# Optimization experiments

Hardware: AMD Instinct MI355X
Metric: run time of the kernel (lower is better)

The kernel has to match this reference:

```python
import jax, jax.numpy as jnp
import numpy as np

B, S, D = 2, 1024, 4096
N_HEADS, KV_HEADS, HEAD_DIM = 32, 8, 128
EPS = 1e-6
ROPE_THETA = 1e6


def setup_inputs() -> dict:
    key = jax.random.key(0)
    ks = jax.random.split(key, 7)
    scale = 0.02
    x = jax.random.normal(ks[0], (B, S, D), dtype=jnp.float32)
    positions = jnp.broadcast_to(jnp.arange(S, dtype=jnp.int32)[None, :], (B, S))
    wq = jax.random.normal(ks[1], (D, N_HEADS, HEAD_DIM), dtype=jnp.float32) * scale
    wk = jax.random.normal(ks[2], (D, KV_HEADS, HEAD_DIM), dtype=jnp.float32) * scale
    wv = jax.random.normal(ks[3], (D, KV_HEADS, HEAD_DIM), dtype=jnp.float32) * scale
    wo = jax.random.normal(ks[4], (N_HEADS, HEAD_DIM, D), dtype=jnp.float32) * scale
    q_norm_w = 1.0 + jax.random.normal(ks[5], (HEAD_DIM,), dtype=jnp.float32) * 0.01
    k_norm_w = 1.0 + jax.random.normal(ks[6], (HEAD_DIM,), dtype=jnp.float32) * 0.01
    return {"x": x, "positions": positions, "wq": wq, "wk": wk, "wv": wv,
            "wo": wo, "q_norm_w": q_norm_w, "k_norm_w": k_norm_w}


def _rms_norm(t, w):
    # per-head RMSNorm over last (head_dim) axis
    var = jnp.mean(jnp.square(t), axis=-1, keepdims=True)
    return (t * jax.lax.rsqrt(var + EPS)) * w


def _rope(t, positions):
    # neox-style rotary embedding; t: [B, S, n, H], positions: [B, S]
    half = t.shape[-1] // 2
    inv_freq = 1.0 / (ROPE_THETA ** (jnp.arange(0, half, dtype=jnp.float32) / half))
    ang = positions.astype(jnp.float32)[..., None] * inv_freq  # [B, S, half]
    cos = jnp.cos(ang)[:, :, None, :]  # [B, S, 1, half]
    sin = jnp.sin(ang)[:, :, None, :]
    t1, t2 = t[..., :half], t[..., half:]
    return jnp.concatenate([t1 * cos - t2 * sin, t2 * cos + t1 * sin], axis=-1)


def reference(x, positions, wq, wk, wv, wo, q_norm_w, k_norm_w):
    # QKV projections (einsum layers: 'bsd,dnh->bsnh')
    q = jnp.einsum('bsd,dnh->bsnh', x, wq)  # [B, S, N, H]
    k = jnp.einsum('bsd,dkh->bskh', x, wk)  # [B, S, K, H]
    v = jnp.einsum('bsd,dkh->bskh', x, wv)
    # per-head QK RMSNorm, then RoPE
    q = _rope(_rms_norm(q, q_norm_w), positions)
    k = _rope(_rms_norm(k, k_norm_w), positions)
    # GQA: expand KV heads to query heads
    groups = N_HEADS // KV_HEADS
    k = jnp.repeat(k, groups, axis=2)  # [B, S, N, H]
    v = jnp.repeat(v, groups, axis=2)
    sm_scale = HEAD_DIM ** -0.5
    scores = jnp.einsum('bqnh,btnh->bnqt', q, k) * sm_scale  # [B, N, S, S]
    causal = jnp.tril(jnp.ones((S, S), dtype=bool))
    scores = jnp.where(causal[None, None], scores, jnp.finfo(scores.dtype).min)
    probs = jax.nn.softmax(scores, axis=-1)
    attn = jnp.einsum('bnqt,btnh->bqnh', probs, v)  # [B, S, N, H]
    out = jnp.einsum('bqnh,nhd->bqd', attn, wo)  # output projection
    return out
```

## Files before the change

kernel.cpp:

```cpp
#include <hip/hip_runtime.h>
#include <stdint.h>

#define S_LEN   1024
#define D_MODEL 4096
#define NHQ     32
#define NKV     8
#define HD      128
#define NTOK    2048
#define NQKV    6144
#define SM_SCALE 0.08838834764831843f
#define LOG2E    1.4426950408889634f

typedef __attribute__((ext_vector_type(8))) __bf16 bf16x8;
typedef __attribute__((ext_vector_type(4))) float f32x4;

__device__ __forceinline__ unsigned short f2bf(float f) {
  union { float f; unsigned u; } x; x.f = f;
  unsigned r = x.u + 0x7fffu + ((x.u >> 16) & 1u);
  return (unsigned short)(r >> 16);
}
__device__ __forceinline__ float bf2f(unsigned short u) {
  union { unsigned u; float f; } x; x.u = (unsigned)u << 16; return x.f;
}

__device__ __forceinline__ void gload_lds16(const void* g, void* l) {
  __builtin_amdgcn_global_load_lds((__attribute__((address_space(1))) void*)g,
                                   (__attribute__((address_space(3))) void*)l,
                                   16, 0, 0);
}

__global__ void k_f32_to_bf16(const float* __restrict__ in,
                              unsigned short* __restrict__ out, int n8) {
  int i = blockIdx.x * blockDim.x + threadIdx.x;
  if (i >= n8) return;
  const float4* p = (const float4*)(in + (size_t)i * 8);
  float4 v0 = p[0], v1 = p[1];
  uint4 o;
  o.x = f2bf(v0.x) | ((unsigned)f2bf(v0.y) << 16);
  o.y = f2bf(v0.z) | ((unsigned)f2bf(v0.w) << 16);
  o.z = f2bf(v1.x) | ((unsigned)f2bf(v1.y) << 16);
  o.w = f2bf(v1.z) | ((unsigned)f2bf(v1.w) << 16);
  *(uint4*)(out + (size_t)i * 8) = o;
}

__global__ void k_transpose(const float* __restrict__ in,
                            unsigned short* __restrict__ out, int R, int C) {
  __shared__ float t[32][33];
  int c = threadIdx.x & 31, r0 = threadIdx.x >> 5;
  int cb = blockIdx.x * 32, rb = blockIdx.y * 32;
#pragma unroll
  for (int i = 0; i < 4; ++i) {
    int r = r0 + i * 8;
    t[r][c] = in[(size_t)(rb + r) * C + cb + c];
  }
  __syncthreads();
#pragma unroll
  for (int i = 0; i < 4; ++i) {
    int r = r0 + i * 8;
    out[(size_t)(cb + r) * R + rb + c] = f2bf(t[c][r]);
  }
}


#define LGKM0 { asm volatile("s_waitcnt lgkmcnt(0)" ::: "memory"); \
                __builtin_amdgcn_sched_barrier(0); }
#define SCHED __builtin_amdgcn_sched_barrier(0);
#define BAR   __builtin_amdgcn_s_barrier();
#define GATE  { if constexpr (NF == 4)                                          \
                  asm volatile("s_waitcnt vmcnt(4)" ::: "memory");              \
                else                                                            \
                  asm volatile("s_waitcnt vmcnt(3)" ::: "memory"); }

#define STGA(h, bufb, kOff)                                                     \
  _Pragma("unroll")                                                             \
  for (int i_ = 0; i_ < 2; ++i_)                                                \
    gload_lds16(gA[i_] + (kOff) + (h) * 64,                                     \
                smem + (bufb) + (h) * 16384 + dA[i_]);

#define STGB(h, bufb, kOff)                                                     \
  _Pragma("unroll")                                                             \
  for (int i_ = 0; i_ < NF / 2; ++i_)                                           \
    gload_lds16(gB[i_] + (kOff) + (h) * 64,                                     \
                smem + (bufb) + 32768 + (h) * (NF * 4096) + dB[i_]);

#define RD_A(dst, mh, kh, bufb)                                                 \
  _Pragma("unroll")                                                             \
  for (int mf = 0; mf < 4; ++mf) {                                              \
    int row = wr * 128 + (mh) * 64 + mf * 16 + lr;                              \
    dst[mf] = *(const bf16x8*)(smem + (bufb) + (kh) * 16384 + row * 64          \
                               + ((lg * 16) ^ (((row >> 1) & 3) << 4)));        \
  }

#define RD_B(dst, kh, bufb)                                                     \
  _Pragma("unroll")                                                             \
  for (int nf = 0; nf < NF; ++nf) {                                             \
    int row = wc * (NF * 16) + nf * 16 + lr;                                    \
    dst[nf] = *(const bf16x8*)(smem + (bufb) + 32768 + (kh) * (NF * 4096)       \
                               + row * 64 + ((lg * 16) ^ (((row >> 1) & 3) << 4))); \
  }

#define MFMA16(mh, AF, BF)                                                      \
  __builtin_amdgcn_s_setprio(1);                                                \
  _Pragma("unroll")                                                             \
  for (int mf = 0; mf < 4; ++mf)                                                \
    _Pragma("unroll")                                                           \
    for (int nf = 0; nf < NF; ++nf)                                             \
      acc[(mh) * 4 + mf][nf] = __builtin_amdgcn_mfma_f32_16x16x32_bf16(         \
          AF[mf], BF[nf], acc[(mh) * 4 + mf][nf], 0, 0, 0);                     \
  __builtin_amdgcn_s_setprio(0);

template <int NF, typename OutT>
__global__ __launch_bounds__(512, 1) void k_gemm256(
    const unsigned short* __restrict__ Aptr,
    const unsigned short* __restrict__ Bptr,
    OutT* __restrict__ C,
    int Kstride, int ldc, int NT, int SGN, int nxn) {
  extern __shared__ __align__(16) char smem[];
  constexpr int BUFST = 32768 + NF * 8192;
  int tid = threadIdx.x;
  int l = tid & 63;
  int w = tid >> 6;
  int lr = l & 15, lg = l >> 4;
  int wr = w >> 2, wc = w & 3;
  int per_xcd = gridDim.x >> 3;
  int x8 = blockIdx.x & 7, i = blockIdx.x >> 3;
  int SGM = per_xcd / SGN;
  int xr = x8 / nxn, xc = x8 - xr * nxn;
  int iy = i / SGN;
  int by = xr * SGM + iy, bx = xc * SGN + (i - iy * SGN);
  int bm = by * 256, bn = bx * (NF * 64);

  const char* gA[2]; int dA[2];
#pragma unroll
  for (int i_ = 0; i_ < 2; ++i_) {
    int lin = i_ * 512 + tid;
    int r_ = lin >> 2, slot = lin & 3, sw = slot ^ ((r_ >> 1) & 3);
    gA[i_] = (const char*)(Aptr + (size_t)(bm + r_) * Kstride) + sw * 16;
    dA[i_] = lin * 16;
  }
  const char* gB[NF / 2]; int dB[NF / 2];
#pragma unroll
  for (int i_ = 0; i_ < NF / 2; ++i_) {
    int lin = i_ * 512 + tid;
    int r_ = lin >> 2, slot = lin & 3, sw = slot ^ ((r_ >> 1) & 3);
    gB[i_] = (const char*)(Bptr + (size_t)(bn + r_) * Kstride) + sw * 16;
    dB[i_] = lin * 16;
  }

  f32x4 acc[8][NF] = {};
  bf16x8 afA[4], afB[4], bfA[NF], bfB[NF];

  STGA(0, 0, 0) STGB(0, 0, 0)
  STGA(1, 0, 0) STGB(1, 0, 0)
  GATE
  BAR
  RD_A(afA, 0, 0, 0) RD_B(bfA, 0, 0)

  for (int kt = 0; kt < NT; ++kt) {
    int curb = (kt & 1) * BUFST;
    int nxtb = BUFST - curb;
    int kOff = (kt + 1) * 128;
    STGA(0, nxtb, kOff)
    BAR LGKM0
    RD_A(afB, 1, 0, curb) SCHED
    MFMA16(0, afA, bfA)
    BAR
    STGB(0, nxtb, kOff)
    GATE BAR LGKM0
    RD_A(afA, 0, 1, curb) RD_B(bfB, 1, curb) SCHED
    MFMA16(1, afB, bfA)
    BAR
    STGA(1, nxtb, kOff)
    BAR LGKM0
    RD_A(afB, 1, 1, curb) SCHED
    MFMA16(0, afA, bfB)
    BAR
    STGB(1, nxtb, kOff)
    GATE BAR LGKM0
    RD_A(afA, 0, 0, nxtb) RD_B(bfA, 0, nxtb) SCHED
    MFMA16(1, afB, bfB)
    BAR
  }

#pragma unroll
  for (int mh = 0; mh < 2; ++mh)
#pragma unroll
    for (int mf = 0; mf < 4; ++mf)
#pragma unroll
      for (int nf = 0; nf < NF; ++nf)
#pragma unroll
        for (int j = 0; j < 4; ++j) {
          size_t idx = (size_t)(bm + wr * 128 + mh * 64 + mf * 16 + lg * 4 + j) * ldc +
                       bn + wc * (NF * 16) + nf * 16 + lr;
          float v = acc[mh * 4 + mf][nf][j];
          if constexpr (sizeof(OutT) == 2) C[idx] = f2bf(v);
          else C[idx] = v;
        }
}

__global__ void k_norm_rope(const unsigned short* __restrict__ qkv,
                            const float* __restrict__ w,
                            const int* __restrict__ positions,
                            unsigned short* __restrict__ out, int nheads, int colbase,
                            float oscale) {
  int wid = blockIdx.x * 4 + (threadIdx.x >> 6);
  int lane = threadIdx.x & 63;
  int token = wid / nheads, head = wid - token * nheads;
  const unsigned short* src = qkv + (size_t)token * NQKV + colbase + head * HD;
  float e0 = bf2f(src[lane]), e1 = bf2f(src[lane + 64]);
  float ss = e0 * e0 + e1 * e1;
#pragma unroll
  for (int m = 1; m < 64; m <<= 1) ss += __shfl_xor(ss, m, 64);
  float rs = rsqrtf(ss * (1.0f / 128.0f) + 1e-6f);
  float n0 = e0 * rs * w[lane], n1 = e1 * rs * w[lane + 64];
  int pos = positions[token];
  float invf = exp2f((float)lane * (-19.931568569324174f / 64.0f));
  float ang = (float)pos * invf;
  float sv, cv;
  sincosf(ang, &sv, &cv);
  float o0 = (n0 * cv - n1 * sv) * oscale;
  float o1 = (n1 * cv + n0 * sv) * oscale;
  int b = token >> 10, s = token & 1023;
  size_t ob = ((size_t)(b * nheads + head) * S_LEN + s) * HD;
  out[ob + lane] = f2bf(o0);
  out[ob + 64 + lane] = f2bf(o1);
}

__global__ void k_v_transpose(const unsigned short* __restrict__ qkv,
                              unsigned short* __restrict__ vt) {
  __shared__ unsigned short t[32][33];
  int slice = blockIdx.z;
  int b = slice >> 3, kh = slice & 7;
  const unsigned short* in = qkv + (size_t)(b * S_LEN) * NQKV + 5120 + kh * HD;
  unsigned short* out = vt + (size_t)slice * HD * S_LEN;
  int c = threadIdx.x & 31, r0 = threadIdx.x >> 5;
  int s0 = blockIdx.y * 32, d0 = blockIdx.x * 32;
#pragma unroll
  for (int i = 0; i < 4; ++i) {
    int r = r0 + i * 8;
    t[r][c] = in[(size_t)(s0 + r) * NQKV + d0 + c];
  }
  __syncthreads();
#pragma unroll
  for (int i = 0; i < 4; ++i) {
    int r = r0 + i * 8;
    out[(size_t)(d0 + r) * S_LEN + s0 + c] = t[c][r];
  }
}

__global__ __launch_bounds__(512) void k_attn(const unsigned short* __restrict__ qh,
                                              const unsigned short* __restrict__ kbuf,
                                              const unsigned short* __restrict__ vtbuf,
                                              unsigned short* __restrict__ attn_out) {
  __shared__ __align__(16) unsigned short k_lds[64 * 128];
  __shared__ __align__(16) unsigned short v_lds[128 * 64];
  __shared__ __align__(16) unsigned short p_lds[8][16 * 64];
  int b = blockIdx.z, h = blockIdx.y, bx = blockIdx.x;
  int khd = h >> 2;
  int tid = threadIdx.x, w = tid >> 6, l = tid & 63;
  int lr = l & 15, lg = l >> 4;
  const unsigned short* K = kbuf + (size_t)(b * NKV + khd) * S_LEN * HD;
  const unsigned short* VT = vtbuf + (size_t)(b * NKV + khd) * HD * S_LEN;
  char* klp = (char*)k_lds;
  char* vlp = (char*)v_lds;
  char* plp = (char*)p_lds[w];
  int swz = (lr & 7) << 4;

  for (int strip = 0; strip < 2; ++strip) {
    int qs = strip ? (7 - bx) : bx;
    int q0 = qs * 128;
    int rbase = q0 + w * 16;
    const unsigned short* Q = qh + ((size_t)(b * NHQ + h) * S_LEN + rbase) * HD;
    bf16x8 qf[4];
#pragma unroll
    for (int kk = 0; kk < 4; ++kk)
      qf[kk] = *(const bf16x8*)&Q[(size_t)lr * HD + kk * 32 + lg * 8];

    f32x4 o[8] = {};
    float m_[4], l_[4];
#pragma unroll
    for (int j = 0; j < 4; ++j) { m_[j] = -1e30f; l_[j] = 0.0f; }

    int nt = 2 * qs + 2;
    for (int t = 0; t < nt; ++t) {
      int t0 = t * 64;
      __syncthreads();
#pragma unroll
      for (int it = 0; it < 2; ++it) {
        int db = (tid + it * 512) * 16;
        int kr = db >> 8, kc = db & 255;
        gload_lds16(K + (size_t)(t0 + kr) * HD + ((kc ^ ((kr & 7) << 4)) >> 1), klp + db);
        int vr = db >> 7, vc = db & 127;
        gload_lds16(VT + (size_t)vr * S_LEN + t0 + ((vc ^ ((vr & 7) << 4)) >> 1), vlp + db);
      }
      __syncthreads();

      f32x4 sc[4];
      __builtin_amdgcn_s_setprio(1);
#pragma unroll
      for (int ct = 0; ct < 4; ++ct) {
        f32x4 s = {};
        int row = ct * 16 + lr;
#pragma unroll
        for (int kk = 0; kk < 4; ++kk) {
          bf16x8 kf = *(const bf16x8*)(klp + row * 256 + ((kk * 64 + lg * 16) ^ swz));
          s = __builtin_amdgcn_mfma_f32_16x16x32_bf16(qf[kk], kf, s, 0, 0, 0);
        }
        sc[ct] = s;
      }
      __builtin_amdgcn_s_setprio(0);

      bool fullw = (t0 + 63 <= rbase);
      float alpha[4];
#pragma unroll
      for (int j = 0; j < 4; ++j) {
        if (!fullw) {
          int rg = rbase + lg * 4 + j;
#pragma unroll
          for (int ct = 0; ct < 4; ++ct)
            sc[ct][j] = (t0 + ct * 16 + lr <= rg) ? sc[ct][j] : -1e30f;
        }
        float mx = fmaxf(fmaxf(sc[0][j], sc[1][j]), fmaxf(sc[2][j], sc[3][j]));
#pragma unroll
        for (int msk = 1; msk < 16; msk <<= 1) mx = fmaxf(mx, __shfl_xor(mx, msk, 64));
        float mn = fmaxf(m_[j], mx);
        alpha[j] = exp2f(m_[j] - mn);
        int q = lg * 4 + j;
        int psw = (q & 7) << 4;
        float ps = 0.0f;
#pragma unroll
        for (int ct = 0; ct < 4; ++ct) {
          float p = exp2f(sc[ct][j] - mn);
          ps += p;
          *(unsigned short*)(plp + q * 128 + (((ct * 16 + lr) * 2) ^ psw)) = f2bf(p);
        }
#pragma unroll
        for (int msk = 1; msk < 16; msk <<= 1) ps += __shfl_xor(ps, msk, 64);
        l_[j] = l_[j] * alpha[j] + ps;
        m_[j] = mn;
      }
#pragma unroll
      for (int dc = 0; dc < 8; ++dc) {
        o[dc][0] *= alpha[0]; o[dc][1] *= alpha[1];
        o[dc][2] *= alpha[2]; o[dc][3] *= alpha[3];
      }
      asm volatile("s_waitcnt lgkmcnt(0)" ::: "memory");
      __builtin_amdgcn_s_setprio(1);
#pragma unroll
      for (int kt = 0; kt < 2; ++kt) {
        bf16x8 pa = *(const bf16x8*)(plp + lr * 128 + ((kt * 64 + lg * 16) ^ swz));
#pragma unroll
        for (int dc = 0; dc < 8; ++dc) {
          int vrow = dc * 16 + lr;
          bf16x8 vf = *(const bf16x8*)(vlp + vrow * 128 + ((kt * 64 + lg * 16) ^ swz));
          o[dc] = __builtin_amdgcn_mfma_f32_16x16x32_bf16(pa, vf, o[dc], 0, 0, 0);
        }
      }
      __builtin_amdgcn_s_setprio(0);
    }

#pragma unroll
    for (int j = 0; j < 4; ++j) {
      int rg = rbase + lg * 4 + j;
      size_t row = (size_t)(b * S_LEN + rg) * D_MODEL + h * HD;
      float inv = 1.0f / l_[j];
#pragma unroll
      for (int dc = 0; dc < 8; ++dc)
        attn_out[row + dc * 16 + lr] = f2bf(o[dc][j] * inv);
    }
  }
}

extern "C" void kernel_launch(void* const* d_in, const int* in_sizes, int n_in,
                              void* d_out, int out_size, void* d_ws, size_t ws_size,
                              hipStream_t stream) {
  const float* x        = (const float*)d_in[0];
  const int* positions  = (const int*)d_in[1];
  const float* wq       = (const float*)d_in[2];
  const float* wk       = (const float*)d_in[3];
  const float* wv       = (const float*)d_in[4];
  const float* wo       = (const float*)d_in[5];
  const float* qnw      = (const float*)d_in[6];
  const float* knw      = (const float*)d_in[7];
  float* out            = (float*)d_out;

  char* ws = (char*)d_ws;
  unsigned short* xb   = (unsigned short*)(ws);
  unsigned short* wB   = (unsigned short*)(ws + 16777216);
  unsigned short* woT  = (unsigned short*)(ws + 67108864);
  unsigned short* qkvb = (unsigned short*)(ws + 100663296);
  unsigned short* qh   = wB;
  unsigned short* khb  = (unsigned short*)(ws + 33554432);
  unsigned short* vtb  = (unsigned short*)(ws + 37748736);
  unsigned short* attn = xb;

  dim3 tb(256);
  k_f32_to_bf16<<<4096, tb, 0, stream>>>(x, xb, 1048576);
  k_transpose<<<dim3(128, 128), tb, 0, stream>>>(wq, wB, 4096, 4096);
  k_transpose<<<dim3(32, 128), tb, 0, stream>>>(wk, wB + (size_t)4096 * 4096, 4096, 1024);
  k_transpose<<<dim3(32, 128), tb, 0, stream>>>(wv, wB + (size_t)5120 * 4096, 4096, 1024);
  k_transpose<<<dim3(128, 128), tb, 0, stream>>>(wo, woT, 4096, 4096);

  k_gemm256<4, unsigned short><<<dim3(192), dim3(512), 131072, stream>>>(
      xb, wB, qkvb, 4096, 6144, 64, 6, 4);

  k_norm_rope<<<16384, tb, 0, stream>>>(qkvb, qnw, positions, qh, 32, 0, SM_SCALE * LOG2E);
  k_norm_rope<<<4096, tb, 0, stream>>>(qkvb, knw, positions, khb, 8, 4096, 1.0f);
  k_v_transpose<<<dim3(4, 32, 16), tb, 0, stream>>>(qkvb, vtb);

  k_attn<<<dim3(4, 32, 2), dim3(512), 0, stream>>>(qh, khb, vtb, attn);

  k_gemm256<2, float><<<dim3(256), dim3(512), 98304, stream>>>(
      attn, woT, out, 4096, 4096, 64, 8, 4);
}
```

Baseline: 331.8 us.

## Fuse prep and norm kernels, split-K the output projection with NF=4 tiles

Merges the x conversion and the four weight transposes into a single launch, and merges the Q/K norm-rope kernels with the V transpose into another. The output projection switches to 256x256 tiles split across two K halves, with the second half written to an fp32 partial buffer and summed by a new reduce kernel. The aim is fewer kernel launches and a better tile shape for the final GEMM, at the cost of extra partial-buffer traffic and an added reduction pass. The K-loop prefetch offset is also clamped so the last iteration does not read past its K range.

```diff
diff --git a/kernel.cpp b/kernel.cpp
--- a/kernel.cpp
+++ b/kernel.cpp
@@ -29,25 +29,33 @@
                                    16, 0, 0);
 }
 
-__global__ void k_f32_to_bf16(const float* __restrict__ in,
-                              unsigned short* __restrict__ out, int n8) {
-  int i = blockIdx.x * blockDim.x + threadIdx.x;
-  if (i >= n8) return;
-  const float4* p = (const float4*)(in + (size_t)i * 8);
-  float4 v0 = p[0], v1 = p[1];
-  uint4 o;
-  o.x = f2bf(v0.x) | ((unsigned)f2bf(v0.y) << 16);
-  o.y = f2bf(v0.z) | ((unsigned)f2bf(v0.w) << 16);
-  o.z = f2bf(v1.x) | ((unsigned)f2bf(v1.y) << 16);
-  o.w = f2bf(v1.z) | ((unsigned)f2bf(v1.w) << 16);
-  *(uint4*)(out + (size_t)i * 8) = o;
-}
-
-__global__ void k_transpose(const float* __restrict__ in,
-                            unsigned short* __restrict__ out, int R, int C) {
+__global__ void k_prep(const float* __restrict__ x,
+                       const float* __restrict__ wq, const float* __restrict__ wk,
+                       const float* __restrict__ wv, const float* __restrict__ wo,
+                       unsigned short* __restrict__ xb,
+                       unsigned short* __restrict__ wB,
+                       unsigned short* __restrict__ woT) {
   __shared__ float t[32][33];
-  int c = threadIdx.x & 31, r0 = threadIdx.x >> 5;
-  int cb = blockIdx.x * 32, rb = blockIdx.y * 32;
+  int bx = blockIdx.x, by = blockIdx.y, tid = threadIdx.x;
+  if (bx >= 320) {
+    int i = ((bx - 320) * 128 + by) * 256 + tid;
+    const float4* p = (const float4*)(x + (size_t)i * 8);
+    float4 v0 = p[0], v1 = p[1];
+    uint4 o;
+    o.x = f2bf(v0.x) | ((unsigned)f2bf(v0.y) << 16);
+    o.y = f2bf(v0.z) | ((unsigned)f2bf(v0.w) << 16);
+    o.z = f2bf(v1.x) | ((unsigned)f2bf(v1.y) << 16);
+    o.w = f2bf(v1.z) | ((unsigned)f2bf(v1.w) << 16);
+    *(uint4*)(xb + (size_t)i * 8) = o;
+    return;
+  }
+  const float* in; unsigned short* out; int C, tbx;
+  if (bx < 128)      { in = wq; out = wB;                          C = 4096; tbx = bx; }
+  else if (bx < 160) { in = wk; out = wB + (size_t)4096 * 4096;    C = 1024; tbx = bx - 128; }
+  else if (bx < 192) { in = wv; out = wB + (size_t)5120 * 4096;    C = 1024; tbx = bx - 160; }
+  else               { in = wo; out = woT;                         C = 4096; tbx = bx - 192; }
+  int c = tid & 31, r0 = tid >> 5;
+  int cb = tbx * 32, rb = by * 32;
 #pragma unroll
   for (int i = 0; i < 4; ++i) {
     int r = r0 + i * 8;
@@ -57,7 +65,7 @@
 #pragma unroll
   for (int i = 0; i < 4; ++i) {
     int r = r0 + i * 8;
-    out[(size_t)(cb + r) * R + rb + c] = f2bf(t[c][r]);
+    out[(size_t)(cb + r) * 4096 + rb + c] = f2bf(t[c][r]);
   }
 }
 
@@ -113,8 +121,8 @@
 __global__ __launch_bounds__(512, 1) void k_gemm256(
     const unsigned short* __restrict__ Aptr,
     const unsigned short* __restrict__ Bptr,
-    OutT* __restrict__ C,
-    int Kstride, int ldc, int NT, int SGN, int nxn) {
+    OutT* __restrict__ C, float* __restrict__ Cpart,
+    int Kstride, int ldc, int NT, int SGN, int nxn, int nps) {
   extern __shared__ __align__(16) char smem[];
   constexpr int BUFST = 32768 + NF * 8192;
   int tid = threadIdx.x;
@@ -122,20 +130,23 @@
   int w = tid >> 6;
   int lr = l & 15, lg = l >> 4;
   int wr = w >> 2, wc = w & 3;
-  int per_xcd = gridDim.x >> 3;
-  int x8 = blockIdx.x & 7, i = blockIdx.x >> 3;
+  int ks = (blockIdx.x >= nps) ? 1 : 0;
+  int bid = blockIdx.x - ks * nps;
+  int per_xcd = nps >> 3;
+  int x8 = bid & 7, i = bid >> 3;
   int SGM = per_xcd / SGN;
   int xr = x8 / nxn, xc = x8 - xr * nxn;
   int iy = i / SGN;
   int by = xr * SGM + iy, bx = xc * SGN + (i - iy * SGN);
   int bm = by * 256, bn = bx * (NF * 64);
+  int k0e = ks * NT * 64;
 
   const char* gA[2]; int dA[2];
 #pragma unroll
   for (int i_ = 0; i_ < 2; ++i_) {
     int lin = i_ * 512 + tid;
     int r_ = lin >> 2, slot = lin & 3, sw = slot ^ ((r_ >> 1) & 3);
-    gA[i_] = (const char*)(Aptr + (size_t)(bm + r_) * Kstride) + sw * 16;
+    gA[i_] = (const char*)(Aptr + (size_t)(bm + r_) * Kstride + k0e) + sw * 16;
     dA[i_] = lin * 16;
   }
   const char* gB[NF / 2]; int dB[NF / 2];
@@ -143,7 +154,7 @@
   for (int i_ = 0; i_ < NF / 2; ++i_) {
     int lin = i_ * 512 + tid;
     int r_ = lin >> 2, slot = lin & 3, sw = slot ^ ((r_ >> 1) & 3);
-    gB[i_] = (const char*)(Bptr + (size_t)(bn + r_) * Kstride) + sw * 16;
+    gB[i_] = (const char*)(Bptr + (size_t)(bn + r_) * Kstride + k0e) + sw * 16;
     dB[i_] = lin * 16;
   }
 
@@ -159,7 +170,8 @@
   for (int kt = 0; kt < NT; ++kt) {
     int curb = (kt & 1) * BUFST;
     int nxtb = BUFST - curb;
-    int kOff = (kt + 1) * 128;
+    int kcl = (kt + 1 < NT) ? kt + 1 : NT - 1;
+    int kOff = kcl * 128;
     STGA(0, nxtb, kOff)
     BAR LGKM0
     RD_A(afB, 1, 0, curb) SCHED
@@ -193,58 +205,82 @@
           size_t idx = (size_t)(bm + wr * 128 + mh * 64 + mf * 16 + lg * 4 + j) * ldc +
                        bn + wc * (NF * 16) + nf * 16 + lr;
           float v = acc[mh * 4 + mf][nf][j];
-          if constexpr (sizeof(OutT) == 2) C[idx] = f2bf(v);
+          if (ks) Cpart[idx] = v;
+          else if constexpr (sizeof(OutT) == 2) C[idx] = f2bf(v);
           else C[idx] = v;
         }
 }
 
-__global__ void k_norm_rope(const unsigned short* __restrict__ qkv,
-                            const float* __restrict__ w,
-                            const int* __restrict__ positions,
-                            unsigned short* __restrict__ out, int nheads, int colbase,
-                            float oscale) {
-  int wid = blockIdx.x * 4 + (threadIdx.x >> 6);
-  int lane = threadIdx.x & 63;
-  int token = wid / nheads, head = wid - token * nheads;
-  const unsigned short* src = qkv + (size_t)token * NQKV + colbase + head * HD;
-  float e0 = bf2f(src[lane]), e1 = bf2f(src[lane + 64]);
-  float ss = e0 * e0 + e1 * e1;
-#pragma unroll
-  for (int m = 1; m < 64; m <<= 1) ss += __shfl_xor(ss, m, 64);
-  float rs = rsqrtf(ss * (1.0f / 128.0f) + 1e-6f);
-  float n0 = e0 * rs * w[lane], n1 = e1 * rs * w[lane + 64];
-  int pos = positions[token];
-  float invf = exp2f((float)lane * (-19.931568569324174f / 64.0f));
-  float ang = (float)pos * invf;
-  float sv, cv;
-  sincosf(ang, &sv, &cv);
-  float o0 = (n0 * cv - n1 * sv) * oscale;
-  float o1 = (n1 * cv + n0 * sv) * oscale;
-  int b = token >> 10, s = token & 1023;
-  size_t ob = ((size_t)(b * nheads + head) * S_LEN + s) * HD;
-  out[ob + lane] = f2bf(o0);
-  out[ob + 64 + lane] = f2bf(o1);
-}
-
-__global__ void k_v_transpose(const unsigned short* __restrict__ qkv,
-                              unsigned short* __restrict__ vt) {
-  __shared__ unsigned short t[32][33];
-  int slice = blockIdx.z;
+__global__ void k_reduce_add(float* __restrict__ out, const float* __restrict__ p,
+                             int n4) {
+  int i = blockIdx.x * blockDim.x + threadIdx.x;
+  int stride = gridDim.x * blockDim.x;
+  for (; i < n4; i += stride) {
+    float4 a = ((const float4*)out)[i];
+    float4 b = ((const float4*)p)[i];
+    a.x += b.x; a.y += b.y; a.z += b.z; a.w += b.w;
+    ((float4*)out)[i] = a;
+  }
+}
+
+__global__ void k_norm_vt(const unsigned short* __restrict__ qkv,
+                          const float* __restrict__ qw,
+                          const float* __restrict__ kw,
+                          const int* __restrict__ positions,
+                          unsigned short* __restrict__ qh,
+                          unsigned short* __restrict__ khb,
+                          unsigned short* __restrict__ vt,
+                          float qscale) {
+  __shared__ unsigned short tt[32][33];
+  int tid = threadIdx.x;
+  if (blockIdx.x < 20480) {
+    int wid = blockIdx.x * 4 + (tid >> 6);
+    int lane = tid & 63;
+    int token = wid / 40, hh = wid - token * 40;
+    bool isq = hh < 32;
+    int head = isq ? hh : hh - 32;
+    int colbase = isq ? head * HD : 4096 + head * HD;
+    const float* w = isq ? qw : kw;
+    float oscale = isq ? qscale : 1.0f;
+    const unsigned short* src = qkv + (size_t)token * NQKV + colbase;
+    float e0 = bf2f(src[lane]), e1 = bf2f(src[lane + 64]);
+    float ss = e0 * e0 + e1 * e1;
+#pragma unroll
+    for (int m = 1; m < 64; m <<= 1) ss += __shfl_xor(ss, m, 64);
+    float rs = rsqrtf(ss * (1.0f / 128.0f) + 1e-6f);
+    float n0 = e0 * rs * w[lane], n1 = e1 * rs * w[lane + 64];
+    int pos = positions[token];
+    float invf = exp2f((float)lane * (-19.931568569324174f / 64.0f));
+    float ang = (float)pos * invf;
+    float sv, cv;
+    sincosf(ang, &sv, &cv);
+    float o0 = (n0 * cv - n1 * sv) * oscale;
+    float o1 = (n1 * cv + n0 * sv) * oscale;
+    int b = token >> 10, s = token & 1023;
+    unsigned short* dst = isq ? qh + ((size_t)(b * NHQ + head) * S_LEN + s) * HD
+                              : khb + ((size_t)(b * NKV + head) * S_LEN + s) * HD;
+    dst[lane] = f2bf(o0);
+    dst[64 + lane] = f2bf(o1);
+    return;
+  }
+  int r = blockIdx.x - 20480;
+  int dx = r & 3, rest = r >> 2;
+  int sy = rest & 31, slice = rest >> 5;
   int b = slice >> 3, kh = slice & 7;
   const unsigned short* in = qkv + (size_t)(b * S_LEN) * NQKV + 5120 + kh * HD;
   unsigned short* out = vt + (size_t)slice * HD * S_LEN;
-  int c = threadIdx.x & 31, r0 = threadIdx.x >> 5;
-  int s0 = blockIdx.y * 32, d0 = blockIdx.x * 32;
+  int c = tid & 31, r0 = tid >> 5;
+  int s0 = sy * 32, d0 = dx * 32;
 #pragma unroll
   for (int i = 0; i < 4; ++i) {
-    int r = r0 + i * 8;
-    t[r][c] = in[(size_t)(s0 + r) * NQKV + d0 + c];
+    int rr = r0 + i * 8;
+    tt[rr][c] = in[(size_t)(s0 + rr) * NQKV + d0 + c];
   }
   __syncthreads();
 #pragma unroll
   for (int i = 0; i < 4; ++i) {
-    int r = r0 + i * 8;
-    out[(size_t)(d0 + r) * S_LEN + s0 + c] = t[c][r];
+    int rr = r0 + i * 8;
+    out[(size_t)(d0 + rr) * S_LEN + s0 + c] = tt[c][rr];
   }
 }
 
@@ -393,23 +429,20 @@
   unsigned short* khb  = (unsigned short*)(ws + 33554432);
   unsigned short* vtb  = (unsigned short*)(ws + 37748736);
   unsigned short* attn = xb;
+  float*          part = (float*)(ws + 16777216);
 
   dim3 tb(256);
-  k_f32_to_bf16<<<4096, tb, 0, stream>>>(x, xb, 1048576);
-  k_transpose<<<dim3(128, 128), tb, 0, stream>>>(wq, wB, 4096, 4096);
-  k_transpose<<<dim3(32, 128), tb, 0, stream>>>(wk, wB + (size_t)4096 * 4096, 4096, 1024);
-  k_transpose<<<dim3(32, 128), tb, 0, stream>>>(wv, wB + (size_t)5120 * 4096, 4096, 1024);
-  k_transpose<<<dim3(128, 128), tb, 0, stream>>>(wo, woT, 4096, 4096);
+  k_prep<<<dim3(352, 128), tb, 0, stream>>>(x, wq, wk, wv, wo, xb, wB, woT);
 
   k_gemm256<4, unsigned short><<<dim3(192), dim3(512), 131072, stream>>>(
-      xb, wB, qkvb, 4096, 6144, 64, 6, 4);
-
-  k_norm_rope<<<16384, tb, 0, stream>>>(qkvb, qnw, positions, qh, 32, 0, SM_SCALE * LOG2E);
-  k_norm_rope<<<4096, tb, 0, stream>>>(qkvb, knw, positions, khb, 8, 4096, 1.0f);
-  k_v_transpose<<<dim3(4, 32, 16), tb, 0, stream>>>(qkvb, vtb);
+      xb, wB, qkvb, nullptr, 4096, 6144, 64, 6, 4, 192);
+
+  k_norm_vt<<<22528, tb, 0, stream>>>(qkvb, qnw, knw, positions, qh, khb, vtb,
+                                      SM_SCALE * LOG2E);
 
   k_attn<<<dim3(4, 32, 2), dim3(512), 0, stream>>>(qh, khb, vtb, attn);
 
-  k_gemm256<2, float><<<dim3(256), dim3(512), 98304, stream>>>(
-      attn, woT, out, 4096, 4096, 64, 8, 4);
-}
+  k_gemm256<4, float><<<dim3(256), dim3(512), 131072, stream>>>(
+      attn, woT, out, part, 4096, 4096, 32, 4, 4, 128);
+  k_reduce_add<<<2048, tb, 0, stream>>>(out, part, 2097152);
+}
```

Result: slower. 340.7 us (+2.7%).
